# Kernel tuning notes

Hardware: AMD Instinct MI355X
Metric: run time of the kernel (lower is better)

## Reference

```python
import jax, jax.numpy as jnp
import numpy as np

B, S, E, H = 4, 2048, 1024, 16
HD = E // H  # 64


def setup_inputs() -> dict:
    key = jax.random.key(0)
    k1, k2, k3, k4, k5 = jax.random.split(key, 5)
    scale = 0.02
    return {
        "hidden_states": jax.random.normal(k1, (B, S, E), dtype=jnp.float32),
        "c_attn_w": jax.random.normal(k2, (E, 3 * E), dtype=jnp.float32) * scale,
        "c_attn_b": jnp.zeros((3 * E,), dtype=jnp.float32),
        "c_proj_w": jax.random.normal(k3, (E, E), dtype=jnp.float32) * scale,
        "c_proj_b": jnp.zeros((E,), dtype=jnp.float32),
    }


def reference(hidden_states, c_attn_w, c_attn_b, c_proj_w, c_proj_b):
    b, s, e = hidden_states.shape
    h, hd = H, HD
    # Conv1D: x @ W + b
    qkv = hidden_states @ c_attn_w + c_attn_b                     # [B,S,3E]
    # Faithful to source: split heads BEFORE splitting q/k/v
    qkv = qkv.reshape(b, s, h, 3 * hd).transpose(0, 2, 1, 3)      # [B,H,S,3*hd]
    q, k, v = jnp.split(qkv, 3, axis=-1)                          # each [B,H,S,hd]
    scores = jnp.einsum("bhqd,bhkd->bhqk", q, k) / (hd ** 0.5)    # [B,H,S,S]
    causal = jnp.tril(jnp.ones((s, s), dtype=bool))
    masked_bias = jnp.asarray(-10000.0, dtype=scores.dtype)
    scores = jnp.where(causal, scores, masked_bias)
    attn_weights = jax.nn.softmax(scores, axis=-1)                # [B,H,S,S]
    attn_out = jnp.einsum("bhqk,bhkd->bhqd", attn_weights, v)     # [B,H,S,hd]
    attn_out = attn_out.transpose(0, 2, 1, 3).reshape(b, s, e)    # merge heads
    out = attn_out @ c_proj_w + c_proj_b                          # [B,S,E]
    return out
```

## Files before the change

kernel.cpp:

```cpp
#include <hip/hip_runtime.h>

typedef __attribute__((ext_vector_type(8))) __bf16 bf16x8;
typedef __attribute__((ext_vector_type(2))) __bf16 bf16x2;
typedef __attribute__((ext_vector_type(8))) unsigned short u16x8;
typedef __attribute__((ext_vector_type(4))) float f32x4;
typedef __attribute__((ext_vector_type(16))) float f32x16;
typedef __attribute__((ext_vector_type(4))) unsigned int u32x4;
typedef unsigned short u16;
typedef unsigned int u32;

constexpr int Bb = 4, Ss = 2048, Ee = 1024, Hh = 16, HDd = 64;
constexpr int Mm = Bb * Ss;
constexpr int N3 = 3 * Ee;
constexpr float QSC = 0.18033688011112042f;
constexpr int BHSTRIDE = Ss * HDd;
constexpr float M0 = 8.0f;

__device__ __forceinline__ u16 f2bf(float f) {
  u32 u = __builtin_bit_cast(u32, f);
  u = (u + 0x7FFFu + ((u >> 16) & 1u)) >> 16;
  return (u16)u;
}
__device__ __forceinline__ u32 pk2(float a, float b) {
  bf16x2 t;
  t[0] = (__bf16)a;
  t[1] = (__bf16)b;
  return __builtin_bit_cast(u32, t);
}
__device__ __forceinline__ float ex2(float x) { return __builtin_exp2f(x); }

__device__ __forceinline__ void gload_lds16(const void* g, void* l) {
  __builtin_amdgcn_global_load_lds(
      (__attribute__((address_space(1))) void*)g,
      (__attribute__((address_space(3))) void*)l, 16, 0, 0);
}

__device__ __forceinline__ f32x4 mfma16(bf16x8 a, bf16x8 b, f32x4 c) {
  return __builtin_amdgcn_mfma_f32_16x16x32_bf16(a, b, c, 0, 0, 0);
}
__device__ __forceinline__ f32x16 mfma32(bf16x8 a, bf16x8 b, f32x16 c) {
  return __builtin_amdgcn_mfma_f32_32x32x16_bf16(a, b, c, 0, 0, 0);
}

__global__ void cast_x_kernel(const float* __restrict__ x, u16* __restrict__ xb, int n4) {
  int i = blockIdx.x * blockDim.x + threadIdx.x;
  int stride = gridDim.x * blockDim.x;
  for (; i < n4; i += stride) {
    float4 v = reinterpret_cast<const float4*>(x)[i];
    ushort4 o;
    o.x = f2bf(v.x); o.y = f2bf(v.y); o.z = f2bf(v.z); o.w = f2bf(v.w);
    reinterpret_cast<ushort4*>(xb)[i] = o;
  }
}

__global__ void transpose_cast_kernel(const float* __restrict__ W, u16* __restrict__ Wt,
                                      int K, int N) {
  __shared__ float tile[32][33];
  int n0 = blockIdx.x * 32, k0 = blockIdx.y * 32;
  int tx = threadIdx.x & 31, ty = threadIdx.x >> 5;
#pragma unroll
  for (int i = 0; i < 4; ++i)
    tile[ty + i * 8][tx] = W[(size_t)(k0 + ty + i * 8) * N + n0 + tx];
  __syncthreads();
#pragma unroll
  for (int i = 0; i < 4; ++i)
    Wt[(size_t)(n0 + ty + i * 8) * K + k0 + tx] = f2bf(tile[tx][ty + i * 8]);
}

__global__ __launch_bounds__(256) void gemm_qkv_kernel(
    const u16* __restrict__ A, const u16* __restrict__ Bt,
    const float* __restrict__ bias,
    u16* __restrict__ Qr, u16* __restrict__ Kp, u16* __restrict__ Vp, int K) {
  extern __shared__ __attribute__((aligned(16))) char smem[];
  u16* ldsA = (u16*)smem;
  u16* ldsB = (u16*)(smem + 8192);
  u16* ldsO = (u16*)smem;

  int tid = threadIdx.x;
  int lane = tid & 63, w = tid >> 6;
  int wr = w >> 1, wc = w & 1;
  int m0 = blockIdx.y * 128, n0 = blockIdx.x * 128;
  const f32x4 fz = {0.f, 0.f, 0.f, 0.f};
  f32x4 acc[4][4];
#pragma unroll
  for (int mi = 0; mi < 4; ++mi)
#pragma unroll
    for (int nj = 0; nj < 4; ++nj) acc[mi][nj] = fz;

  int srow = tid >> 2;
  int scol = (tid & 3) * 8;
  const u16* aptr = A + (size_t)(m0 + srow) * K + scol;
  const u16* bptr = Bt + (size_t)(n0 + srow) * K + scol;
  u16* la = &ldsA[srow * 32 + scol];
  u16* lb = &ldsB[srow * 32 + scol];

  for (int k0 = 0; k0 < K; k0 += 32) {
    gload_lds16(aptr + k0, la);
    gload_lds16(aptr + k0 + (size_t)64 * K, la + 64 * 32);
    gload_lds16(bptr + k0, lb);
    gload_lds16(bptr + k0 + (size_t)64 * K, lb + 64 * 32);
    __syncthreads();
    bf16x8 af[4], bfr[4];
#pragma unroll
    for (int mi = 0; mi < 4; ++mi)
      af[mi] = *(const bf16x8*)&ldsA[(wr * 64 + mi * 16 + (lane & 15)) * 32 + (lane >> 4) * 8];
#pragma unroll
    for (int nj = 0; nj < 4; ++nj)
      bfr[nj] = *(const bf16x8*)&ldsB[(wc * 64 + nj * 16 + (lane & 15)) * 32 + (lane >> 4) * 8];
#pragma unroll
    for (int mi = 0; mi < 4; ++mi)
#pragma unroll
      for (int nj = 0; nj < 4; ++nj)
        acc[mi][nj] = mfma16(af[mi], bfr[nj], acc[mi][nj]);
    __syncthreads();
  }

  int gi0 = n0 >> 6;
  {
    int typ = (gi0 + wc) % 3;
    float cs = (typ == 0) ? QSC : 1.0f;
#pragma unroll
    for (int mi = 0; mi < 4; ++mi)
#pragma unroll
      for (int nj = 0; nj < 4; ++nj) {
        int dl = nj * 16 + (lane & 15);
        float bn = bias[n0 + wc * 64 + dl];
#pragma unroll
        for (int r = 0; r < 4; ++r) {
          int ml = wr * 64 + mi * 16 + (lane >> 4) * 4 + r;
          ldsO[(wc * 128 + ml) * 72 + dl] = f2bf((acc[mi][nj][r] + bn) * cs);
        }
      }
  }
  __syncthreads();

  int b = m0 >> 11;
  int mrow0 = m0 & 2047;
#pragma unroll
  for (int g = 0; g < 2; ++g) {
    int gi = gi0 + g;
    int typ = gi % 3;
    int h = gi / 3;
    size_t basebh = (size_t)(b * 16 + h) * BHSTRIDE;
    if (typ == 2) {
#pragma unroll
      for (int i = 0; i < 4; ++i) {
        int c = tid + 256 * i;
        int dl = c & 63, s64 = (c >> 6) & 1, kv8 = c >> 7;
        u16x8 val;
        int lrow = g * 128 + s64 * 64 + kv8 * 8;
#pragma unroll
        for (int e = 0; e < 8; ++e) val[e] = ldsO[(lrow + e) * 72 + dl];
        int tile = (mrow0 >> 6) + s64;
        size_t off = basebh + (size_t)tile * 4096 + (dl >> 5) * 2048 +
                     (kv8 >> 1) * 512 + (kv8 & 1) * 256 + (dl & 31) * 8;
        *(u16x8*)(Vp + off) = val;
      }
    } else {
#pragma unroll
      for (int i = 0; i < 4; ++i) {
        int c = tid + 256 * i;
        int sl = c >> 3, dc = c & 7;
        u16x8 val = *(const u16x8*)&ldsO[(g * 128 + sl) * 72 + dc * 8];
        int srw = mrow0 + sl;
        if (typ == 0) {
          *(u16x8*)(Qr + basebh + (size_t)srw * 64 + dc * 8) = val;
        } else {
          int tile = srw >> 6, rl = srw & 63;
          size_t off = basebh + (size_t)tile * 4096 + (rl >> 5) * 2048 +
                       (dc >> 1) * 512 + (dc & 1) * 256 + (rl & 31) * 8;
          *(u16x8*)(Kp + off) = val;
        }
      }
    }
  }
}

__global__ __launch_bounds__(256) void gemm_kernel(
    const u16* __restrict__ A, const u16* __restrict__ Bt,
    const float* __restrict__ bias, float* __restrict__ Cout,
    int M, int N, int K) {
  __shared__ __attribute__((aligned(16))) u16 ldsA[128 * 32];
  __shared__ __attribute__((aligned(16))) u16 ldsB[128 * 32];
  int tid = threadIdx.x;
  int lane = tid & 63, w = tid >> 6;
  int wr = w >> 1, wc = w & 1;
  int m0 = blockIdx.y * 128, n0 = blockIdx.x * 128;
  const f32x4 fz = {0.f, 0.f, 0.f, 0.f};
  f32x4 acc[4][4];
#pragma unroll
  for (int mi = 0; mi < 4; ++mi)
#pragma unroll
    for (int nj = 0; nj < 4; ++nj) acc[mi][nj] = fz;

  int srow = tid >> 2;
  int scol = (tid & 3) * 8;
  const u16* aptr = A + (size_t)(m0 + srow) * K + scol;
  const u16* bptr = Bt + (size_t)(n0 + srow) * K + scol;
  u16* la = &ldsA[srow * 32 + scol];
  u16* lb = &ldsB[srow * 32 + scol];

  for (int k0 = 0; k0 < K; k0 += 32) {
    gload_lds16(aptr + k0, la);
    gload_lds16(aptr + k0 + (size_t)64 * K, la + 64 * 32);
    gload_lds16(bptr + k0, lb);
    gload_lds16(bptr + k0 + (size_t)64 * K, lb + 64 * 32);
    __syncthreads();
    bf16x8 af[4], bfr[4];
#pragma unroll
    for (int mi = 0; mi < 4; ++mi)
      af[mi] = *(const bf16x8*)&ldsA[(wr * 64 + mi * 16 + (lane & 15)) * 32 + (lane >> 4) * 8];
#pragma unroll
    for (int nj = 0; nj < 4; ++nj)
      bfr[nj] = *(const bf16x8*)&ldsB[(wc * 64 + nj * 16 + (lane & 15)) * 32 + (lane >> 4) * 8];
#pragma unroll
    for (int mi = 0; mi < 4; ++mi)
#pragma unroll
      for (int nj = 0; nj < 4; ++nj)
        acc[mi][nj] = mfma16(af[mi], bfr[nj], acc[mi][nj]);
    __syncthreads();
  }

#pragma unroll
  for (int mi = 0; mi < 4; ++mi) {
#pragma unroll
    for (int nj = 0; nj < 4; ++nj) {
      int n = n0 + wc * 64 + nj * 16 + (lane & 15);
      float bn = bias[n];
#pragma unroll
      for (int r = 0; r < 4; ++r) {
        int m = m0 + wr * 64 + mi * 16 + (lane >> 4) * 4 + r;
        Cout[(size_t)m * N + n] = acc[mi][nj][r] + bn;
      }
    }
  }
}

__global__ __launch_bounds__(256) void attn_kernel(const u16* __restrict__ Qr,
                                                   const u16* __restrict__ Kp,
                                                   const u16* __restrict__ Vp,
                                                   u16* __restrict__ aout) {
  __shared__ float mbuf[2][64][33];

  int bh = blockIdx.x;
  int j = gridDim.y - 1 - blockIdx.y;
  int tid = threadIdx.x, w = tid >> 6, lane = tid & 63;
  int hi = lane >> 5, ln31 = lane & 31;
  int qrow = 32 * j + ln31;
  int nt = (j >> 1) + 1;
  int par = (j & 1) ? 32 : 0;

  size_t basebh = (size_t)bh * BHSTRIDE;
  const u16* kp = Kp + basebh + (size_t)w * 4096 + hi * 256 + ln31 * 8;
  const u16* vp = Vp + basebh + (size_t)w * 4096 + hi * 256 + ln31 * 8;

  bf16x8 qf[4];
#pragma unroll
  for (int kc = 0; kc < 4; ++kc)
    qf[kc] = *(const bf16x8*)(Qr + basebh + (size_t)qrow * 64 + kc * 16 + hi * 8);

  f32x16 o[2];
#pragma unroll
  for (int dm = 0; dm < 2; ++dm)
#pragma unroll
    for (int e = 0; e < 16; ++e) o[dm][e] = 0.f;
  float lrun = 0.f;

  for (int t = w; t < nt; t += 4, kp += 4 * 4096, vp += 4 * 4096) {
    bf16x8 kf[2][4], vf[2][4];
#pragma unroll
    for (int mt = 0; mt < 2; ++mt)
#pragma unroll
      for (int kc = 0; kc < 4; ++kc)
        kf[mt][kc] = *(const bf16x8*)(kp + mt * 2048 + kc * 512);
#pragma unroll
    for (int dm = 0; dm < 2; ++dm)
#pragma unroll
      for (int kw = 0; kw < 4; ++kw)
        vf[dm][kw] = *(const bf16x8*)(vp + dm * 2048 + kw * 512);

    f32x16 sc[2];
#pragma unroll
    for (int mt = 0; mt < 2; ++mt)
#pragma unroll
      for (int e = 0; e < 16; ++e) sc[mt][e] = 0.f;
    __builtin_amdgcn_s_setprio(1);
#pragma unroll
    for (int mt = 0; mt < 2; ++mt)
#pragma unroll
      for (int kc = 0; kc < 4; ++kc)
        sc[mt] = mfma32(kf[mt][kc], qf[kc], sc[mt]);
    __builtin_amdgcn_s_setprio(0);

    if (t == nt - 1) {
#pragma unroll
      for (int mt = 0; mt < 2; ++mt)
#pragma unroll
        for (int r = 0; r < 16; ++r) {
          bool msk = (32 * mt + (r & 3) + 8 * (r >> 2) + 4 * hi) > (ln31 + par);
          sc[mt][r] = msk ? -__builtin_inff() : sc[mt][r];
        }
    }
    float s0a = 0.f, s1a = 0.f, s2a = 0.f, s3a = 0.f;
#pragma unroll
    for (int mt = 0; mt < 2; ++mt)
#pragma unroll
      for (int r = 0; r < 16; ++r) {
        float e = ex2(sc[mt][r] - M0);
        sc[mt][r] = e;
        if ((r & 3) == 0) s0a += e;
        else if ((r & 3) == 1) s1a += e;
        else if ((r & 3) == 2) s2a += e;
        else s3a += e;
      }
    float sum = (s0a + s1a) + (s2a + s3a);
    sum += __shfl_xor(sum, 32);
    lrun += sum;

#pragma unroll
    for (int kw = 0; kw < 4; ++kw) {
      int mt = kw >> 1, k8 = (kw & 1) * 8;
      u32 a0 = pk2(sc[mt][k8 + 0], sc[mt][k8 + 1]);
      u32 a1 = pk2(sc[mt][k8 + 2], sc[mt][k8 + 3]);
      u32 b0 = pk2(sc[mt][k8 + 4], sc[mt][k8 + 5]);
      u32 b1 = pk2(sc[mt][k8 + 6], sc[mt][k8 + 7]);
      u32 s0 = hi ? a0 : b0;
      u32 s1 = hi ? a1 : b1;
      u32 r0 = (u32)__shfl_xor((int)s0, 32);
      u32 r1 = (u32)__shfl_xor((int)s1, 32);
      u32x4 fw;
      fw.x = hi ? r0 : a0;
      fw.y = hi ? r1 : a1;
      fw.z = hi ? b0 : r0;
      fw.w = hi ? b1 : r1;
      bf16x8 pf = __builtin_bit_cast(bf16x8, fw);
      __builtin_amdgcn_s_setprio(1);
#pragma unroll
      for (int dm = 0; dm < 2; ++dm)
        o[dm] = mfma32(vf[dm][kw], pf, o[dm]);
      __builtin_amdgcn_s_setprio(0);
    }
  }

  if (w >= 2) {
    mbuf[w - 2][lane][0] = lrun;
#pragma unroll
    for (int dm = 0; dm < 2; ++dm)
#pragma unroll
      for (int e = 0; e < 16; ++e) mbuf[w - 2][lane][1 + dm * 16 + e] = o[dm][e];
  }
  __syncthreads();
  if (w < 2) {
    lrun += mbuf[w][lane][0];
#pragma unroll
    for (int dm = 0; dm < 2; ++dm)
#pragma unroll
      for (int e = 0; e < 16; ++e) o[dm][e] += mbuf[w][lane][1 + dm * 16 + e];
  }
  __syncthreads();
  if (w == 1) {
    mbuf[0][lane][0] = lrun;
#pragma unroll
    for (int dm = 0; dm < 2; ++dm)
#pragma unroll
      for (int e = 0; e < 16; ++e) mbuf[0][lane][1 + dm * 16 + e] = o[dm][e];
  }
  __syncthreads();
  if (w == 0) {
    lrun += mbuf[0][lane][0];
#pragma unroll
    for (int dm = 0; dm < 2; ++dm)
#pragma unroll
      for (int e = 0; e < 16; ++e) o[dm][e] += mbuf[0][lane][1 + dm * 16 + e];
    int b = bh >> 4, h = bh & 15;
    float inv = 1.f / lrun;
    u16* orow = aout + (size_t)(b * Ss + qrow) * Ee + h * HDd;
#pragma unroll
    for (int dm = 0; dm < 2; ++dm)
#pragma unroll
      for (int g = 0; g < 4; ++g) {
        ushort4 st;
        st.x = f2bf(o[dm][4 * g + 0] * inv);
        st.y = f2bf(o[dm][4 * g + 1] * inv);
        st.z = f2bf(o[dm][4 * g + 2] * inv);
        st.w = f2bf(o[dm][4 * g + 3] * inv);
        *(ushort4*)(orow + 32 * dm + 8 * g + 4 * hi) = st;
      }
  }
}

extern "C" void kernel_launch(void* const* d_in, const int* in_sizes, int n_in,
                              void* d_out, int out_size, void* d_ws, size_t ws_size,
                              hipStream_t stream) {
  const float* hs        = (const float*)d_in[0];
  const float* c_attn_w  = (const float*)d_in[1];
  const float* c_attn_b  = (const float*)d_in[2];
  const float* c_proj_w  = (const float*)d_in[3];
  const float* c_proj_b  = (const float*)d_in[4];
  float* out = (float*)d_out;

  char* ws = (char*)d_ws;
  size_t off = 0;
  u16* xb     = (u16*)(ws + off); off += (size_t)Mm * Ee * 2;
  u16* wqkvt  = (u16*)(ws + off); off += (size_t)N3 * Ee * 2;
  u16* wprojt = (u16*)(ws + off); off += (size_t)Ee * Ee * 2;
  u16* Qr     = (u16*)(ws + off); off += (size_t)64 * BHSTRIDE * 2;
  u16* Kp     = (u16*)(ws + off); off += (size_t)64 * BHSTRIDE * 2;
  u16* Vp     = (u16*)(ws + off); off += (size_t)64 * BHSTRIDE * 2;
  u16* aoutb  = (u16*)(ws + off); off += (size_t)Mm * Ee * 2;
  if (ws_size < off) return;

  (void)hipFuncSetAttribute(reinterpret_cast<const void*>(gemm_qkv_kernel),
                            hipFuncAttributeMaxDynamicSharedMemorySize, 36864);

  cast_x_kernel<<<2048, 256, 0, stream>>>(hs, xb, Mm * Ee / 4);
  transpose_cast_kernel<<<dim3(N3 / 32, Ee / 32), 256, 0, stream>>>(c_attn_w, wqkvt, Ee, N3);
  transpose_cast_kernel<<<dim3(Ee / 32, Ee / 32), 256, 0, stream>>>(c_proj_w, wprojt, Ee, Ee);
  gemm_qkv_kernel<<<dim3(N3 / 128, Mm / 128), 256, 36864, stream>>>(
      xb, wqkvt, c_attn_b, Qr, Kp, Vp, Ee);
  attn_kernel<<<dim3(Bb * Hh, 64), 256, 0, stream>>>(Qr, Kp, Vp, aoutb);
  gemm_kernel<<<dim3(Ee / 128, Mm / 128), 256, 0, stream>>>(
      aoutb, wprojt, c_proj_b, out, Mm, Ee, Ee);
}
```

Before: 188.4 us.

## Rewrite QKV GEMM with 256x256 tiles, double-buffered swizzled LDS, and phased MFMA

Replaces the 128x128 single-buffered QKV projection GEMM with a 512-thread 256x256-tile kernel using K-step 64. The kernel double-buffers A/B tiles in LDS, uses an XOR swizzle to avoid bank conflicts, interleaves prefetch of the next tile with MFMA phases, and raises wave priority during MFMA bursts. A block-index swizzle groups blocks for L2 reuse. The aim is more operand reuse per byte loaded and better overlap of loads with compute. In exchange it uses 128KB of LDS and runs one block per CU, and the epilogue is split into two passes.

```diff
diff --git a/kernel.cpp b/kernel.cpp
--- a/kernel.cpp
+++ b/kernel.cpp
@@ -67,112 +67,169 @@
     Wt[(size_t)(n0 + ty + i * 8) * K + k0 + tx] = f2bf(tile[tx][ty + i * 8]);
 }
 
-__global__ __launch_bounds__(256) void gemm_qkv_kernel(
+__global__ __launch_bounds__(512, 1) void gemm256_qkv(
     const u16* __restrict__ A, const u16* __restrict__ Bt,
     const float* __restrict__ bias,
-    u16* __restrict__ Qr, u16* __restrict__ Kp, u16* __restrict__ Vp, int K) {
-  extern __shared__ __attribute__((aligned(16))) char smem[];
-  u16* ldsA = (u16*)smem;
-  u16* ldsB = (u16*)(smem + 8192);
-  u16* ldsO = (u16*)smem;
-
-  int tid = threadIdx.x;
-  int lane = tid & 63, w = tid >> 6;
-  int wr = w >> 1, wc = w & 1;
-  int m0 = blockIdx.y * 128, n0 = blockIdx.x * 128;
+    u16* __restrict__ Qr, u16* __restrict__ Kp, u16* __restrict__ Vp) {
+  extern __shared__ __attribute__((aligned(16))) u16 dyn[];
+  constexpr int K = 1024, NT = 16;
+
+  int f = blockIdx.x;
+  int swz = (f & 7) * 48 + (f >> 3);
+  int bx = swz % 12, by = swz / 12;
+  int m0 = by * 256, n0 = bx * 256;
+
+  int tid = threadIdx.x, lane = tid & 63, wid = tid >> 6;
+  int wr = wid >> 2, wc = wid & 3;
+  int l7 = lane & 7, l8 = lane >> 3;
+  int swcol = (l7 ^ l8) * 8;
+
+  const u16* Ab = A + (size_t)(m0 + l8) * K + swcol;
+  const u16* Bb = Bt + (size_t)(n0 + l8) * K + swcol;
+
+  f32x4 acc[8][4];
   const f32x4 fz = {0.f, 0.f, 0.f, 0.f};
-  f32x4 acc[4][4];
-#pragma unroll
-  for (int mi = 0; mi < 4; ++mi)
+#pragma unroll
+  for (int mi = 0; mi < 8; ++mi)
 #pragma unroll
     for (int nj = 0; nj < 4; ++nj) acc[mi][nj] = fz;
 
-  int srow = tid >> 2;
-  int scol = (tid & 3) * 8;
-  const u16* aptr = A + (size_t)(m0 + srow) * K + scol;
-  const u16* bptr = Bt + (size_t)(n0 + srow) * K + scol;
-  u16* la = &ldsA[srow * 32 + scol];
-  u16* lb = &ldsB[srow * 32 + scol];
-
-  for (int k0 = 0; k0 < K; k0 += 32) {
-    gload_lds16(aptr + k0, la);
-    gload_lds16(aptr + k0 + (size_t)64 * K, la + 64 * 32);
-    gload_lds16(bptr + k0, lb);
-    gload_lds16(bptr + k0 + (size_t)64 * K, lb + 64 * 32);
-    __syncthreads();
-    bf16x8 af[4], bfr[4];
-#pragma unroll
-    for (int mi = 0; mi < 4; ++mi)
-      af[mi] = *(const bf16x8*)&ldsA[(wr * 64 + mi * 16 + (lane & 15)) * 32 + (lane >> 4) * 8];
-#pragma unroll
-    for (int nj = 0; nj < 4; ++nj)
-      bfr[nj] = *(const bf16x8*)&ldsB[(wc * 64 + nj * 16 + (lane & 15)) * 32 + (lane >> 4) * 8];
-#pragma unroll
-    for (int mi = 0; mi < 4; ++mi)
-#pragma unroll
-      for (int nj = 0; nj < 4; ++nj)
-        acc[mi][nj] = mfma16(af[mi], bfr[nj], acc[mi][nj]);
-    __syncthreads();
-  }
-
-  int gi0 = n0 >> 6;
-  {
-    int typ = (gi0 + wc) % 3;
-    float cs = (typ == 0) ? QSC : 1.0f;
-#pragma unroll
-    for (int mi = 0; mi < 4; ++mi)
+  auto STA = [&](int tt, int c) {
+    int ch = wid * 4 + c;
+    gload_lds16(Ab + (size_t)(ch * 8) * K + tt * 64,
+                dyn + (tt & 1) * 16384 + ch * 512);
+  };
+  auto STB = [&](int tt, int c) {
+    int ch = wid * 4 + c;
+    gload_lds16(Bb + (size_t)(ch * 8) * K + tt * 64,
+                dyn + 32768 + (tt & 1) * 16384 + ch * 512);
+  };
+  auto LDA = [&](const u16* buf, int mi, int ks) -> bf16x8 {
+    int row = wr * 128 + mi * 16 + (lane & 15);
+    int j = ((ks * 4 + (lane >> 4)) ^ l7) * 8;
+    return *(const bf16x8*)&buf[row * 64 + j];
+  };
+  auto LDB = [&](const u16* buf, int ni, int ks) -> bf16x8 {
+    int row = wc * 64 + ni * 16 + (lane & 15);
+    int j = ((ks * 4 + (lane >> 4)) ^ l7) * 8;
+    return *(const bf16x8*)&buf[row * 64 + j];
+  };
+
+#define PHASE_MFMA(miA, miB)                                  \
+  __builtin_amdgcn_s_barrier();                               \
+  asm volatile("s_waitcnt lgkmcnt(0)" ::: "memory");          \
+  __builtin_amdgcn_sched_barrier(0);                          \
+  __builtin_amdgcn_s_setprio(1);                              \
+  _Pragma("unroll")                                           \
+  for (int ni = 0; ni < 4; ++ni) {                            \
+    acc[miA][ni] = mfma16(a00, bfr[ni][0], acc[miA][ni]);     \
+    acc[miA][ni] = mfma16(a01, bfr[ni][1], acc[miA][ni]);     \
+    acc[miB][ni] = mfma16(a10, bfr[ni][0], acc[miB][ni]);     \
+    acc[miB][ni] = mfma16(a11, bfr[ni][1], acc[miB][ni]);     \
+  }                                                           \
+  __builtin_amdgcn_s_setprio(0);
+
+#pragma unroll
+  for (int c = 0; c < 4; ++c) STA(0, c);
+#pragma unroll
+  for (int c = 0; c < 4; ++c) STB(0, c);
+
+  for (int t = 0; t < NT; ++t) {
+    const u16* Ar = dyn + (t & 1) * 16384;
+    const u16* Br = dyn + 32768 + (t & 1) * 16384;
+    bool pre = (t + 1) < NT;
+    asm volatile("s_waitcnt vmcnt(0)" ::: "memory");
+    __builtin_amdgcn_s_barrier();
+
+    bf16x8 bfr[4][2];
+#pragma unroll
+    for (int ni = 0; ni < 4; ++ni) {
+      bfr[ni][0] = LDB(Br, ni, 0);
+      bfr[ni][1] = LDB(Br, ni, 1);
+    }
+    bf16x8 a00 = LDA(Ar, 0, 0), a01 = LDA(Ar, 0, 1);
+    bf16x8 a10 = LDA(Ar, 1, 0), a11 = LDA(Ar, 1, 1);
+    if (pre) { STA(t + 1, 0); STA(t + 1, 1); STA(t + 1, 2); STA(t + 1, 3); }
+    PHASE_MFMA(0, 1)
+
+    a00 = LDA(Ar, 2, 0); a01 = LDA(Ar, 2, 1);
+    a10 = LDA(Ar, 3, 0); a11 = LDA(Ar, 3, 1);
+    if (pre) { STB(t + 1, 0); STB(t + 1, 1); STB(t + 1, 2); STB(t + 1, 3); }
+    PHASE_MFMA(2, 3)
+
+    a00 = LDA(Ar, 4, 0); a01 = LDA(Ar, 4, 1);
+    a10 = LDA(Ar, 5, 0); a11 = LDA(Ar, 5, 1);
+    PHASE_MFMA(4, 5)
+
+    a00 = LDA(Ar, 6, 0); a01 = LDA(Ar, 6, 1);
+    a10 = LDA(Ar, 7, 0); a11 = LDA(Ar, 7, 1);
+    PHASE_MFMA(6, 7)
+  }
+#undef PHASE_MFMA
+  __syncthreads();
+
+  int gi0 = bx * 4;
+  int bb = m0 >> 11;
+  int mrow0 = m0 & 2047;
+#pragma unroll
+  for (int p = 0; p < 2; ++p) {
+    if ((wc >> 1) == p) {
+      int gg = wc & 1;
+      int gi = gi0 + p * 2 + gg;
+      int typ = gi % 3;
+      float cs = (typ == 0) ? QSC : 1.0f;
 #pragma unroll
       for (int nj = 0; nj < 4; ++nj) {
         int dl = nj * 16 + (lane & 15);
-        float bn = bias[n0 + wc * 64 + dl];
-#pragma unroll
-        for (int r = 0; r < 4; ++r) {
-          int ml = wr * 64 + mi * 16 + (lane >> 4) * 4 + r;
-          ldsO[(wc * 128 + ml) * 72 + dl] = f2bf((acc[mi][nj][r] + bn) * cs);
+        float bn = bias[gi * 64 + dl];
+#pragma unroll
+        for (int mi = 0; mi < 8; ++mi)
+#pragma unroll
+          for (int r = 0; r < 4; ++r) {
+            int row = wr * 128 + mi * 16 + (lane >> 4) * 4 + r;
+            dyn[(gg * 256 + row) * 72 + dl] = f2bf((acc[mi][nj][r] + bn) * cs);
+          }
+      }
+    }
+    __syncthreads();
+#pragma unroll
+    for (int gg = 0; gg < 2; ++gg) {
+      int gi = gi0 + p * 2 + gg;
+      int typ = gi % 3, h = gi / 3;
+      size_t basebh = (size_t)(bb * 16 + h) * BHSTRIDE;
+      if (typ == 2) {
+#pragma unroll
+        for (int i = 0; i < 4; ++i) {
+          int c = tid + 512 * i;
+          int dl = c & 63, tsel = (c >> 6) & 3, kv8 = c >> 8;
+          u16x8 val;
+          int lrow = gg * 256 + tsel * 64 + kv8 * 8;
+#pragma unroll
+          for (int e = 0; e < 8; ++e) val[e] = dyn[(lrow + e) * 72 + dl];
+          int tile = (mrow0 >> 6) + tsel;
+          size_t o = basebh + (size_t)tile * 4096 + (dl >> 5) * 2048 +
+                     (kv8 >> 1) * 512 + (kv8 & 1) * 256 + (dl & 31) * 8;
+          *(u16x8*)(Vp + o) = val;
+        }
+      } else {
+#pragma unroll
+        for (int i = 0; i < 4; ++i) {
+          int c = tid + 512 * i;
+          int sl = c >> 3, dc = c & 7;
+          u16x8 val = *(const u16x8*)&dyn[(gg * 256 + sl) * 72 + dc * 8];
+          int srw = mrow0 + sl;
+          if (typ == 0) {
+            *(u16x8*)(Qr + basebh + (size_t)srw * 64 + dc * 8) = val;
+          } else {
+            int tile = srw >> 6, rl = srw & 63;
+            size_t o = basebh + (size_t)tile * 4096 + (rl >> 5) * 2048 +
+                       (dc >> 1) * 512 + (dc & 1) * 256 + (rl & 31) * 8;
+            *(u16x8*)(Kp + o) = val;
+          }
         }
       }
-  }
-  __syncthreads();
-
-  int b = m0 >> 11;
-  int mrow0 = m0 & 2047;
-#pragma unroll
-  for (int g = 0; g < 2; ++g) {
-    int gi = gi0 + g;
-    int typ = gi % 3;
-    int h = gi / 3;
-    size_t basebh = (size_t)(b * 16 + h) * BHSTRIDE;
-    if (typ == 2) {
-#pragma unroll
-      for (int i = 0; i < 4; ++i) {
-        int c = tid + 256 * i;
-        int dl = c & 63, s64 = (c >> 6) & 1, kv8 = c >> 7;
-        u16x8 val;
-        int lrow = g * 128 + s64 * 64 + kv8 * 8;
-#pragma unroll
-        for (int e = 0; e < 8; ++e) val[e] = ldsO[(lrow + e) * 72 + dl];
-        int tile = (mrow0 >> 6) + s64;
-        size_t off = basebh + (size_t)tile * 4096 + (dl >> 5) * 2048 +
-                     (kv8 >> 1) * 512 + (kv8 & 1) * 256 + (dl & 31) * 8;
-        *(u16x8*)(Vp + off) = val;
-      }
-    } else {
-#pragma unroll
-      for (int i = 0; i < 4; ++i) {
-        int c = tid + 256 * i;
-        int sl = c >> 3, dc = c & 7;
-        u16x8 val = *(const u16x8*)&ldsO[(g * 128 + sl) * 72 + dc * 8];
-        int srw = mrow0 + sl;
-        if (typ == 0) {
-          *(u16x8*)(Qr + basebh + (size_t)srw * 64 + dc * 8) = val;
-        } else {
-          int tile = srw >> 6, rl = srw & 63;
-          size_t off = basebh + (size_t)tile * 4096 + (rl >> 5) * 2048 +
-                       (dc >> 1) * 512 + (dc & 1) * 256 + (rl & 31) * 8;
-          *(u16x8*)(Kp + off) = val;
-        }
-      }
-    }
+    }
+    __syncthreads();
   }
 }
 
@@ -410,14 +467,13 @@
   u16* aoutb  = (u16*)(ws + off); off += (size_t)Mm * Ee * 2;
   if (ws_size < off) return;
 
-  (void)hipFuncSetAttribute(reinterpret_cast<const void*>(gemm_qkv_kernel),
-                            hipFuncAttributeMaxDynamicSharedMemorySize, 36864);
+  (void)hipFuncSetAttribute(reinterpret_cast<const void*>(gemm256_qkv),
+                            hipFuncAttributeMaxDynamicSharedMemorySize, 131072);
 
   cast_x_kernel<<<2048, 256, 0, stream>>>(hs, xb, Mm * Ee / 4);
   transpose_cast_kernel<<<dim3(N3 / 32, Ee / 32), 256, 0, stream>>>(c_attn_w, wqkvt, Ee, N3);
   transpose_cast_kernel<<<dim3(Ee / 32, Ee / 32), 256, 0, stream>>>(c_proj_w, wprojt, Ee, Ee);
-  gemm_qkv_kernel<<<dim3(N3 / 128, Mm / 128), 256, 36864, stream>>>(
-      xb, wqkvt, c_attn_b, Qr, Kp, Vp, Ee);
+  gemm256_qkv<<<384, 512, 131072, stream>>>(xb, wqkvt, c_attn_b, Qr, Kp, Vp);
   attn_kernel<<<dim3(Bb * Hh, 64), 256, 0, stream>>>(Qr, Kp, Vp, aoutb);
   gemm_kernel<<<dim3(Ee / 128, Mm / 128), 256, 0, stream>>>(
       aoutb, wprojt, c_proj_b, out, Mm, Ee, Ee);
```

Result: faster. 179.8 us (-4.6%).
